# Kernel optimization log

Hardware: AMD Instinct MI355X
Metric: run time of the kernel (lower is better)

Reference implementation:

```python
import jax, jax.numpy as jnp
import numpy as np

O, I, G = 11008, 4096, 128  # out_features, in_features, weight_group


def setup_inputs() -> dict:
    key = jax.random.key(0)
    k1, k2, k3, k4, k5 = jax.random.split(key, 5)
    x = jax.random.normal(k1, (4096, I), dtype=jnp.float16)
    qweight = jax.random.randint(k2, (O, I * 4 // 8), 0, 256, dtype=jnp.int32)
    weight_scale = (jax.random.uniform(k3, (O, I // G), dtype=jnp.float32) * 0.02 + 0.001).astype(jnp.float16)
    weight_zero = jax.random.randint(k4, (O, I // G), 0, 16, dtype=jnp.int32)
    bias = jax.random.normal(k5, (O,), dtype=jnp.float16)
    return {"x": x, "qweight": qweight, "weight_scale": weight_scale,
            "weight_zero": weight_zero, "bias": bias}


def _dequant_w(qweight, weight_scale, weight_zero):
    # unpack two 4-bit values per byte: low nibble first, then high nibble
    low = qweight & 0xF
    high = (qweight >> 4) & 0xF
    w_q = jnp.stack([low, high], axis=-1).reshape(O, I)  # [O, I] ints in [0,16)
    # per-group dequant: (q - zero) * scale, group size G along in_features
    w = (w_q.astype(jnp.float16).reshape(-1, G)
         - weight_zero.reshape(-1, 1).astype(jnp.float16))
    w = w * weight_scale.reshape(-1, 1)
    return w.reshape(O, I).astype(jnp.float16)


def reference(x, qweight, weight_scale, weight_zero, bias):
    w = _dequant_w(qweight, weight_scale, weight_zero)  # [O, I] fp16
    return x @ w.T + bias  # F.linear(x, w, bias)
```

## Files before the change

kernel.cpp:

```cpp
#include <hip/hip_runtime.h>
#include <stdint.h>

#define MDIM 4096
#define NDIM 11008
#define KDIM 4096
#define KHALF 2048
#define NGRP 32
#define NXCD 8

#define WBYTES ((size_t)NDIM * KDIM * 2)
#define XBYTES ((size_t)MDIM * KDIM * 2)
#define WS_NEED (WBYTES + XBYTES)

#define G_BM 256
#define G_BN 256
#define G_BK 64
#define G_NTH 512
#define G_NTILN (NDIM / G_BN)
#define G_NWG ((MDIM / G_BM) * G_NTILN)

#define F_BM 128
#define F_BN 128
#define F_BK 64
#define F_NTH 256
#define F_NTILN (NDIM / F_BN)
#define F_NWG ((MDIM / F_BM) * F_NTILN)

typedef __attribute__((ext_vector_type(4))) float f32x4;
typedef __attribute__((ext_vector_type(8))) _Float16 f16x8;
typedef __attribute__((ext_vector_type(4))) int i32x4;
typedef __attribute__((ext_vector_type(4))) unsigned int u32x4;

__device__ __forceinline__ unsigned int pk16(float a, float b) {
  return __builtin_bit_cast(unsigned int, __builtin_amdgcn_cvt_pkrtz(a, b));
}
__device__ __forceinline__ unsigned int dq_pair(int qi, float fz, float s) {
  unsigned int q = (unsigned int)qi;
  float f0 = __uint_as_float((q & 0xFu) | 0x4B000000u);
  float f1 = __uint_as_float(((q >> 4) & 0xFu) | 0x4B000000u);
  return pk16((f0 - fz) * s, (f1 - fz) * s);
}
__device__ __forceinline__ void load_lds16(const void* g, void* l) {
  __builtin_amdgcn_global_load_lds(
      (__attribute__((address_space(1))) void*)(void*)g,
      (__attribute__((address_space(3))) void*)l, 16, 0, 0);
}

__global__ void __launch_bounds__(256)
dequant_w(const int* __restrict__ qw, const float* __restrict__ scl,
          const int* __restrict__ zro, _Float16* __restrict__ wh) {
  const unsigned int QTOT = (unsigned int)NDIM * KHALF;
  const unsigned int stride = gridDim.x * blockDim.x;
  for (unsigned int t = blockIdx.x * blockDim.x + threadIdx.x; t * 4u < QTOT;
       t += stride) {
    const unsigned int f = t * 4u;
    const unsigned int n = f >> 11;
    const unsigned int kk = f & (KHALF - 1);
    const unsigned int g = kk >> 6;
    const float s = scl[n * NGRP + g];
    const float fz = __uint_as_float(0x4B000000u | (unsigned int)zro[n * NGRP + g]);
    const i32x4 q = *(const i32x4*)(qw + f);
    u32x4 w;
#pragma unroll
    for (int e = 0; e < 4; ++e) w[e] = dq_pair(q[e], fz, s);
    *(u32x4*)(wh + (size_t)f * 2) = w;
  }
}

__global__ void __launch_bounds__(256)
cvt_x(const float* __restrict__ x, _Float16* __restrict__ xh) {
  const unsigned int XTOT = (unsigned int)MDIM * KDIM;
  const unsigned int stride = gridDim.x * blockDim.x;
  for (unsigned int t = blockIdx.x * blockDim.x + threadIdx.x; t * 8u < XTOT;
       t += stride) {
    const unsigned int f = t * 8u;
    const f32x4 a = *(const f32x4*)(x + f);
    const f32x4 b = *(const f32x4*)(x + f + 4);
    u32x4 w;
    w[0] = pk16(a[0], a[1]);
    w[1] = pk16(a[2], a[3]);
    w[2] = pk16(b[0], b[1]);
    w[3] = pk16(b[2], b[3]);
    *(u32x4*)(xh + f) = w;
  }
}

#define ABUF(b, h) ((b) * 32768 + (h) * 8192)
#define BBUF(b, h) ((b) * 32768 + 16384 + (h) * 8192)

#define BARRIER __builtin_amdgcn_s_barrier()
#define LGK0 do { asm volatile("s_waitcnt lgkmcnt(0)" ::: "memory"); \
                  __builtin_amdgcn_sched_barrier(0); } while (0)
#define VMC4 do { asm volatile("s_waitcnt vmcnt(4)" ::: "memory"); \
                  __builtin_amdgcn_sched_barrier(0); } while (0)

__global__ void __launch_bounds__(G_NTH, 2)
gemm_f16_8ph(const _Float16* __restrict__ xh, const _Float16* __restrict__ wh,
             const float* __restrict__ bia, float* __restrict__ outp) {
  __shared__ _Float16 lds[65536];

  const int tid = threadIdx.x;
  int wg = blockIdx.x;
  wg = (wg & 7) * (G_NWG / 8) + (wg >> 3);
  const int by = wg / G_NTILN;
  const int bx = wg - by * G_NTILN;
  const int m0 = by * G_BM;
  const int n0 = bx * G_BN;

  const int rowL = tid >> 3;
  const int swc = (((tid & 7) ^ (rowL & 7)) << 3);
  const unsigned int aO0 = (unsigned int)(m0 + rowL) * KDIM + swc;
  const unsigned int aO1 = aO0 + (unsigned int)128 * KDIM;
  const unsigned int bO0 = (unsigned int)(n0 + rowL) * KDIM + swc;
  const unsigned int bO1 = bO0 + (unsigned int)128 * KDIM;
  const int dst0 = tid << 3;

#define ST(base_el, gb, thoff, ko)                                     \
  do {                                                                 \
    load_lds16((gb) + (thoff) + (ko), lds + (base_el) + dst0);         \
    load_lds16((gb) + (thoff) + (unsigned)64 * KDIM + (ko),            \
               lds + (base_el) + 4096 + dst0);                         \
  } while (0)

  const int wave = tid >> 6, lane = tid & 63;
  const int wm = wave >> 2, wn = wave & 3;
  const int fr = lane & 15, fq = lane >> 4;
  const int pc0 = (fq ^ (fr & 7)) << 3;
  const int pc1 = ((4 + fq) ^ (fr & 7)) << 3;
  const int aoff0 = fr * 64 + pc0, aoff1 = fr * 64 + pc1;
  const int bb = ((wn & 1) << 12) + fr * 64;
  const int boff0 = bb + pc0, boff1 = bb + pc1;

  const _Float16* aP0 = lds + ABUF(0, 0) + wm * 8192;
  const _Float16* aP1 = lds + ABUF(1, 0) + wm * 8192;
  const _Float16* bP0 = lds + BBUF(0, 0) + (wn >> 1) * 8192;
  const _Float16* bP1 = lds + BBUF(1, 0) + (wn >> 1) * 8192;

#define RD_A03(P)                                           \
  _Pragma("unroll") for (int u = 0; u < 4; ++u) {           \
    aF[u][0] = *(const f16x8*)((P) + u * 1024 + aoff0);     \
    aF[u][1] = *(const f16x8*)((P) + u * 1024 + aoff1);     \
  }
#define RD_A47(P)                                               \
  _Pragma("unroll") for (int u = 0; u < 4; ++u) {               \
    aF[4 + u][0] = *(const f16x8*)((P) + (4 + u) * 1024 + aoff0); \
    aF[4 + u][1] = *(const f16x8*)((P) + (4 + u) * 1024 + aoff1); \
  }
#define RD_B01(P)                                           \
  _Pragma("unroll") for (int v = 0; v < 2; ++v) {           \
    bF[v][0] = *(const f16x8*)((P) + v * 1024 + boff0);     \
    bF[v][1] = *(const f16x8*)((P) + v * 1024 + boff1);     \
  }
#define RD_B23(P)                                               \
  _Pragma("unroll") for (int v = 0; v < 2; ++v) {               \
    bF[2 + v][0] = *(const f16x8*)((P) + (2 + v) * 1024 + boff0); \
    bF[2 + v][1] = *(const f16x8*)((P) + (2 + v) * 1024 + boff1); \
  }
#define QUAD(MI, NI)                                                     \
  do {                                                                   \
    __builtin_amdgcn_s_setprio(1);                                       \
    _Pragma("unroll") for (int u = 0; u < 4; ++u) {                      \
      _Pragma("unroll") for (int v = 0; v < 2; ++v) {                    \
        acc[(MI) + u][(NI) + v] = __builtin_amdgcn_mfma_f32_16x16x32_f16( \
            aF[(MI) + u][0], bF[(NI) + v][0], acc[(MI) + u][(NI) + v], 0, 0, 0); \
        acc[(MI) + u][(NI) + v] = __builtin_amdgcn_mfma_f32_16x16x32_f16( \
            aF[(MI) + u][1], bF[(NI) + v][1], acc[(MI) + u][(NI) + v], 0, 0, 0); \
      }                                                                  \
    }                                                                    \
    __builtin_amdgcn_s_setprio(0);                                       \
  } while (0)

  f16x8 aF[8][2], bF[4][2];
  f32x4 acc[8][4];
  const f32x4 fzero = {0.f, 0.f, 0.f, 0.f};
#pragma unroll
  for (int i = 0; i < 8; ++i)
#pragma unroll
    for (int j = 0; j < 4; ++j) acc[i][j] = fzero;

  ST(ABUF(0, 0), xh, aO0, 0u);
  ST(ABUF(0, 1), xh, aO1, 0u);
  ST(BBUF(0, 0), wh, bO0, 0u);
  ST(BBUF(0, 1), wh, bO1, 0u);
  ST(ABUF(1, 0), xh, aO0, 64u);
  ST(ABUF(1, 1), xh, aO1, 64u);
  VMC4;
  BARRIER;

  for (int it = 0; it < KDIM / 128; ++it) {
    const unsigned int k0 = (unsigned int)it << 7;
    const unsigned int ko1 = k0 + 64;
    const unsigned int ko2 = (k0 + 128) & 4095u;
    const unsigned int ko3 = (k0 + 192) & 4095u;

    RD_A03(aP0); RD_B01(bP0);
    ST(BBUF(1, 0), wh, bO0, ko1);
    BARRIER; LGK0; QUAD(0, 0); BARRIER;
    RD_A47(aP0);
    ST(BBUF(1, 1), wh, bO1, ko1);
    BARRIER; LGK0; QUAD(4, 0); BARRIER;
    RD_B23(bP0);
    ST(ABUF(0, 0), xh, aO0, ko2);
    BARRIER; LGK0; QUAD(0, 2); BARRIER;
    ST(ABUF(0, 1), xh, aO1, ko2);
    BARRIER; LGK0; QUAD(4, 2); VMC4; BARRIER;
    RD_A03(aP1); RD_B01(bP1);
    ST(BBUF(0, 0), wh, bO0, ko2);
    BARRIER; LGK0; QUAD(0, 0); BARRIER;
    RD_A47(aP1);
    ST(BBUF(0, 1), wh, bO1, ko2);
    BARRIER; LGK0; QUAD(4, 0); BARRIER;
    RD_B23(bP1);
    ST(ABUF(1, 0), xh, aO0, ko3);
    BARRIER; LGK0; QUAD(0, 2); BARRIER;
    ST(ABUF(1, 1), xh, aO1, ko3);
    BARRIER; LGK0; QUAD(4, 2); VMC4; BARRIER;
  }

#pragma unroll
  for (int ni = 0; ni < 4; ++ni) {
    const int n = n0 + wn * 64 + ni * 16 + fr;
    const float bv = bia[n];
#pragma unroll
    for (int mi = 0; mi < 8; ++mi) {
      const int m = m0 + wm * 128 + mi * 16 + (fq << 2);
      const size_t base = (size_t)m * NDIM + n;
#pragma unroll
      for (int j = 0; j < 4; ++j)
        outp[base + (size_t)j * NDIM] = acc[mi][ni][j] + bv;
    }
  }
}

__global__ void __launch_bounds__(F_NTH)
wlinear_fused(const float* __restrict__ x, const int* __restrict__ qw,
              const float* __restrict__ scl, const int* __restrict__ zro,
              const float* __restrict__ bia, float* __restrict__ outp) {
  __shared__ _Float16 ldsA[F_BM][F_BK];
  __shared__ _Float16 ldsB[F_BN][F_BK];

  const int tid = threadIdx.x;
  int wg = blockIdx.x;
  wg = (wg & (NXCD - 1)) * (F_NWG / NXCD) + (wg >> 3);
  const int by = wg / F_NTILN;
  const int bx = wg - by * F_NTILN;
  const int m0 = by * F_BM;
  const int n0 = bx * F_BN;

  const int srow = tid >> 1;
  const int sh = tid & 1;
  const int ssw = srow & 7;
  const float* xrow = x + (size_t)(m0 + srow) * KDIM + sh * 32;
  const int* qrow = qw + (size_t)(n0 + srow) * KHALF + sh * 16;
  const float* sclrow = scl + (size_t)(n0 + srow) * NGRP;
  const int* zrow = zro + (size_t)(n0 + srow) * NGRP;

  const int wave = tid >> 6;
  const int lane = tid & 63;
  const int wr = wave >> 1;
  const int wc = wave & 1;
  const int fr = lane & 15;
  const int fq = lane >> 4;
  const int off0 = ((fq ^ (fr & 7)) << 3);

  const f32x4 fzero = {0.f, 0.f, 0.f, 0.f};
  f32x4 acc[4][4];
#pragma unroll
  for (int i = 0; i < 4; ++i)
#pragma unroll
    for (int j = 0; j < 4; ++j) acc[i][j] = fzero;

  f32x4 xv[8];
  i32x4 qv[4];
  {
    const f32x4* xp = (const f32x4*)xrow;
#pragma unroll
    for (int i = 0; i < 8; ++i) xv[i] = xp[i];
    const i32x4* qp = (const i32x4*)qrow;
#pragma unroll
    for (int i = 0; i < 4; ++i) qv[i] = qp[i];
  }
  float s_n = sclrow[0];
  float fz_n = __uint_as_float(0x4B000000u | (unsigned int)zrow[0]);

  for (int k0 = 0; k0 < KDIM; k0 += F_BK) {
    __syncthreads();
#pragma unroll
    for (int j = 0; j < 4; ++j) {
      u32x4 wch;
      wch[0] = pk16(xv[2 * j][0], xv[2 * j][1]);
      wch[1] = pk16(xv[2 * j][2], xv[2 * j][3]);
      wch[2] = pk16(xv[2 * j + 1][0], xv[2 * j + 1][1]);
      wch[3] = pk16(xv[2 * j + 1][2], xv[2 * j + 1][3]);
      const int ps = (sh * 4 + j) ^ ssw;
      *(u32x4*)&ldsA[srow][ps << 3] = wch;
    }
#pragma unroll
    for (int ii = 0; ii < 4; ++ii) {
      u32x4 wch;
#pragma unroll
      for (int e = 0; e < 4; ++e) wch[e] = dq_pair(qv[ii][e], fz_n, s_n);
      const int ps = (sh * 4 + ii) ^ ssw;
      *(u32x4*)&ldsB[srow][ps << 3] = wch;
    }
    if (k0 + F_BK < KDIM) {
      const f32x4* xp = (const f32x4*)(xrow + k0 + F_BK);
#pragma unroll
      for (int i = 0; i < 8; ++i) xv[i] = xp[i];
      const i32x4* qp = (const i32x4*)(qrow + ((k0 + F_BK) >> 1));
#pragma unroll
      for (int i = 0; i < 4; ++i) qv[i] = qp[i];
      const int gn = (k0 + F_BK) >> 7;
      s_n = sclrow[gn];
      fz_n = __uint_as_float(0x4B000000u | (unsigned int)zrow[gn]);
    }
    __syncthreads();

#pragma unroll
    for (int ks = 0; ks < F_BK; ks += 32) {
      const int off = (ks == 0) ? off0 : (off0 ^ 32);
      f16x8 a[4], b[4];
#pragma unroll
      for (int mi = 0; mi < 4; ++mi)
        a[mi] = *(const f16x8*)&ldsA[wr * 64 + mi * 16 + fr][off];
#pragma unroll
      for (int ni = 0; ni < 4; ++ni)
        b[ni] = *(const f16x8*)&ldsB[wc * 64 + ni * 16 + fr][off];
#pragma unroll
      for (int mi = 0; mi < 4; ++mi)
#pragma unroll
        for (int ni = 0; ni < 4; ++ni)
          acc[mi][ni] = __builtin_amdgcn_mfma_f32_16x16x32_f16(
              a[mi], b[ni], acc[mi][ni], 0, 0, 0);
    }
  }

#pragma unroll
  for (int ni = 0; ni < 4; ++ni) {
    const int n = n0 + wc * 64 + ni * 16 + fr;
    const float bv = bia[n];
#pragma unroll
    for (int mi = 0; mi < 4; ++mi) {
      const int m = m0 + wr * 64 + mi * 16 + (fq << 2);
      const size_t base = (size_t)m * NDIM + n;
#pragma unroll
      for (int j = 0; j < 4; ++j)
        outp[base + (size_t)j * NDIM] = acc[mi][ni][j] + bv;
    }
  }
}

extern "C" void kernel_launch(void* const* d_in, const int* in_sizes, int n_in,
                              void* d_out, int out_size, void* d_ws, size_t ws_size,
                              hipStream_t stream) {
  (void)in_sizes; (void)n_in; (void)out_size;
  const float* x = (const float*)d_in[0];
  const int* qw = (const int*)d_in[1];
  const float* scl = (const float*)d_in[2];
  const int* zro = (const int*)d_in[3];
  const float* bia = (const float*)d_in[4];
  float* outp = (float*)d_out;

  if (ws_size >= WS_NEED) {
    _Float16* wh = (_Float16*)d_ws;
    _Float16* xh = (_Float16*)((char*)d_ws + WBYTES);
    dequant_w<<<2048, 256, 0, stream>>>(qw, scl, zro, wh);
    cvt_x<<<1024, 256, 0, stream>>>(x, xh);
    gemm_f16_8ph<<<G_NWG, G_NTH, 0, stream>>>(xh, wh, bia, outp);
  } else {
    wlinear_fused<<<F_NWG, F_NTH, 0, stream>>>(x, qw, scl, zro, bia, outp);
  }
}
```

Measured before the change: 618.4 us.

## Stream packed 4-bit weights into GEMM and dequantize in-kernel to LDS

The full fp16 dequantized weight matrix is no longer materialized. A pre-pass packs the int32-per-byte qweight into dense bytes and packs scale and zero into one word per group. The GEMM then loads those bytes through registers, dequantizes them with packed half arithmetic straight into the swizzled B LDS tiles, and changes the vmcnt waits to match. This removes the large fp16 weight write and re-read, in exchange for VALU dequant work inside the MFMA loop and a register-staged load path in place of direct-to-LDS loads.

```diff
diff --git a/kernel.cpp b/kernel.cpp
--- a/kernel.cpp
+++ b/kernel.cpp
@@ -5,16 +5,17 @@
 #define NDIM 11008
 #define KDIM 4096
 #define KHALF 2048
+#define KBYTES 2048
 #define NGRP 32
 #define NXCD 8
 
-#define WBYTES ((size_t)NDIM * KDIM * 2)
 #define XBYTES ((size_t)MDIM * KDIM * 2)
-#define WS_NEED (WBYTES + XBYTES)
+#define WPBYTES ((size_t)NDIM * KBYTES)
+#define SZBYTES ((size_t)NDIM * NGRP * 4)
+#define WS_NEED (XBYTES + WPBYTES + SZBYTES)
 
 #define G_BM 256
 #define G_BN 256
-#define G_BK 64
 #define G_NTH 512
 #define G_NTILN (NDIM / G_BN)
 #define G_NWG ((MDIM / G_BM) * G_NTILN)
@@ -28,6 +29,7 @@
 
 typedef __attribute__((ext_vector_type(4))) float f32x4;
 typedef __attribute__((ext_vector_type(8))) _Float16 f16x8;
+typedef __attribute__((ext_vector_type(2))) _Float16 h2;
 typedef __attribute__((ext_vector_type(4))) int i32x4;
 typedef __attribute__((ext_vector_type(4))) unsigned int u32x4;
 
@@ -40,6 +42,15 @@
   float f1 = __uint_as_float(((q >> 4) & 0xFu) | 0x4B000000u);
   return pk16((f0 - fz) * s, (f1 - fz) * s);
 }
+__device__ __forceinline__ unsigned int dq_byte(unsigned int w, int bi,
+                                                unsigned int zpk,
+                                                unsigned int spk) {
+  const unsigned int b = (w >> (8 * bi)) & 0xFFu;
+  const unsigned int u = 0x64006400u | (b & 0xFu) | ((b & 0xF0u) << 12);
+  const h2 r = (__builtin_bit_cast(h2, u) - __builtin_bit_cast(h2, zpk)) *
+               __builtin_bit_cast(h2, spk);
+  return __builtin_bit_cast(unsigned int, r);
+}
 __device__ __forceinline__ void load_lds16(const void* g, void* l) {
   __builtin_amdgcn_global_load_lds(
       (__attribute__((address_space(1))) void*)(void*)g,
@@ -47,23 +58,20 @@
 }
 
 __global__ void __launch_bounds__(256)
-dequant_w(const int* __restrict__ qw, const float* __restrict__ scl,
-          const int* __restrict__ zro, _Float16* __restrict__ wh) {
-  const unsigned int QTOT = (unsigned int)NDIM * KHALF;
+pack_w(const int* __restrict__ qw, unsigned char* __restrict__ wp) {
+  const unsigned int TOT = (unsigned int)NDIM * KHALF / 16u;
   const unsigned int stride = gridDim.x * blockDim.x;
-  for (unsigned int t = blockIdx.x * blockDim.x + threadIdx.x; t * 4u < QTOT;
+  for (unsigned int t = blockIdx.x * blockDim.x + threadIdx.x; t < TOT;
        t += stride) {
-    const unsigned int f = t * 4u;
-    const unsigned int n = f >> 11;
-    const unsigned int kk = f & (KHALF - 1);
-    const unsigned int g = kk >> 6;
-    const float s = scl[n * NGRP + g];
-    const float fz = __uint_as_float(0x4B000000u | (unsigned int)zro[n * NGRP + g]);
-    const i32x4 q = *(const i32x4*)(qw + f);
-    u32x4 w;
-#pragma unroll
-    for (int e = 0; e < 4; ++e) w[e] = dq_pair(q[e], fz, s);
-    *(u32x4*)(wh + (size_t)f * 2) = w;
+    const i32x4* qp = (const i32x4*)(qw + (size_t)t * 16);
+    u32x4 o;
+#pragma unroll
+    for (int j = 0; j < 4; ++j) {
+      const i32x4 q = qp[j];
+      o[j] = ((unsigned)q[0] & 0xFFu) | (((unsigned)q[1] & 0xFFu) << 8) |
+             (((unsigned)q[2] & 0xFFu) << 16) | (((unsigned)q[3] & 0xFFu) << 24);
+    }
+    *(u32x4*)(wp + (size_t)t * 16) = o;
   }
 }
 
@@ -85,18 +93,40 @@
   }
 }
 
+__global__ void __launch_bounds__(256)
+pack_sz(const float* __restrict__ scl, const int* __restrict__ zro,
+        unsigned int* __restrict__ szp) {
+  const unsigned int TOT = (unsigned int)NDIM * NGRP / 4u;
+  const unsigned int stride = gridDim.x * blockDim.x;
+  for (unsigned int t = blockIdx.x * blockDim.x + threadIdx.x; t < TOT;
+       t += stride) {
+    const f32x4 s = *(const f32x4*)(scl + (size_t)t * 4);
+    const i32x4 z = *(const i32x4*)(zro + (size_t)t * 4);
+    u32x4 o;
+#pragma unroll
+    for (int j = 0; j < 4; ++j) {
+      const unsigned int sb = pk16(s[j], s[j]) & 0xFFFFu;
+      o[j] = sb | ((unsigned)z[j] << 16);
+    }
+    *(u32x4*)(szp + (size_t)t * 4) = o;
+  }
+}
+
 #define ABUF(b, h) ((b) * 32768 + (h) * 8192)
 #define BBUF(b, h) ((b) * 32768 + 16384 + (h) * 8192)
 
 #define BARRIER __builtin_amdgcn_s_barrier()
 #define LGK0 do { asm volatile("s_waitcnt lgkmcnt(0)" ::: "memory"); \
                   __builtin_amdgcn_sched_barrier(0); } while (0)
-#define VMC4 do { asm volatile("s_waitcnt vmcnt(4)" ::: "memory"); \
-                  __builtin_amdgcn_sched_barrier(0); } while (0)
+#define VMC(N) do { asm volatile("s_waitcnt vmcnt(" #N ")" ::: "memory"); \
+                    __builtin_amdgcn_sched_barrier(0); } while (0)
+#define FENCE do { asm volatile("" ::: "memory"); \
+                   __builtin_amdgcn_sched_barrier(0); } while (0)
 
 __global__ void __launch_bounds__(G_NTH, 2)
-gemm_f16_8ph(const _Float16* __restrict__ xh, const _Float16* __restrict__ wh,
-             const float* __restrict__ bia, float* __restrict__ outp) {
+gemm_w4(const _Float16* __restrict__ xh, const unsigned char* __restrict__ wp,
+        const unsigned int* __restrict__ szp, const float* __restrict__ bia,
+        float* __restrict__ outp) {
   __shared__ _Float16 lds[65536];
 
   const int tid = threadIdx.x;
@@ -111,8 +141,6 @@
   const int swc = (((tid & 7) ^ (rowL & 7)) << 3);
   const unsigned int aO0 = (unsigned int)(m0 + rowL) * KDIM + swc;
   const unsigned int aO1 = aO0 + (unsigned int)128 * KDIM;
-  const unsigned int bO0 = (unsigned int)(n0 + rowL) * KDIM + swc;
-  const unsigned int bO1 = bO0 + (unsigned int)128 * KDIM;
   const int dst0 = tid << 3;
 
 #define ST(base_el, gb, thoff, ko)                                     \
@@ -120,6 +148,23 @@
     load_lds16((gb) + (thoff) + (ko), lds + (base_el) + dst0);         \
     load_lds16((gb) + (thoff) + (unsigned)64 * KDIM + (ko),            \
                lds + (base_el) + 4096 + dst0);                         \
+  } while (0)
+
+  const int nloc = tid >> 1;
+  const int bh = tid & 1;
+  const int nsw = nloc & 7;
+  const unsigned char* bqp = wp + (size_t)(n0 + nloc) * KBYTES + bh * 16;
+  const unsigned int* szr = szp + (size_t)(n0 + nloc) * NGRP;
+
+#define DQW(QV, BUF)                                                      \
+  do {                                                                    \
+    _Pragma("unroll") for (int j = 0; j < 4; ++j) {                       \
+      u32x4 o;                                                            \
+      _Pragma("unroll") for (int bi = 0; bi < 4; ++bi)                    \
+        o[bi] = dq_byte((QV)[j], bi, zpk, spk);                           \
+      *(u32x4*)(lds + (BUF) * 32768 + 16384 + nloc * 64 +                 \
+                ((((bh << 2) + j) ^ nsw) << 3)) = o;                      \
+    }                                                                     \
   } while (0)
 
   const int wave = tid >> 6, lane = tid & 63;
@@ -141,8 +186,8 @@
     aF[u][0] = *(const f16x8*)((P) + u * 1024 + aoff0);     \
     aF[u][1] = *(const f16x8*)((P) + u * 1024 + aoff1);     \
   }
-#define RD_A47(P)                                               \
-  _Pragma("unroll") for (int u = 0; u < 4; ++u) {               \
+#define RD_A47(P)                                                 \
+  _Pragma("unroll") for (int u = 0; u < 4; ++u) {                 \
     aF[4 + u][0] = *(const f16x8*)((P) + (4 + u) * 1024 + aoff0); \
     aF[4 + u][1] = *(const f16x8*)((P) + (4 + u) * 1024 + aoff1); \
   }
@@ -151,8 +196,8 @@
     bF[v][0] = *(const f16x8*)((P) + v * 1024 + boff0);     \
     bF[v][1] = *(const f16x8*)((P) + v * 1024 + boff1);     \
   }
-#define RD_B23(P)                                               \
-  _Pragma("unroll") for (int v = 0; v < 2; ++v) {               \
+#define RD_B23(P)                                                 \
+  _Pragma("unroll") for (int v = 0; v < 2; ++v) {                 \
     bF[2 + v][0] = *(const f16x8*)((P) + (2 + v) * 1024 + boff0); \
     bF[2 + v][1] = *(const f16x8*)((P) + (2 + v) * 1024 + boff1); \
   }
@@ -178,43 +223,65 @@
 #pragma unroll
     for (int j = 0; j < 4; ++j) acc[i][j] = fzero;
 
+  unsigned int zpk = 0, spk = 0;
+
+  u32x4 q0 = *(const u32x4*)(bqp + 0);
+  u32x4 q1 = *(const u32x4*)(bqp + 32);
+  unsigned int szv = szr[0];
+  FENCE;
   ST(ABUF(0, 0), xh, aO0, 0u);
   ST(ABUF(0, 1), xh, aO1, 0u);
-  ST(BBUF(0, 0), wh, bO0, 0u);
-  ST(BBUF(0, 1), wh, bO1, 0u);
   ST(ABUF(1, 0), xh, aO0, 64u);
   ST(ABUF(1, 1), xh, aO1, 64u);
-  VMC4;
+  FENCE;
+  VMC(8);
+  {
+    const unsigned int zl = szv >> 16;
+    zpk = 0x64006400u | zl | (zl << 16);
+    spk = (szv & 0xFFFFu) | (szv << 16);
+    DQW(q0, 0);
+    DQW(q1, 1);
+  }
+  VMC(4);
+  LGK0;
   BARRIER;
 
   for (int it = 0; it < KDIM / 128; ++it) {
-    const unsigned int k0 = (unsigned int)it << 7;
-    const unsigned int ko1 = k0 + 64;
-    const unsigned int ko2 = (k0 + 128) & 4095u;
-    const unsigned int ko3 = (k0 + 192) & 4095u;
+    const unsigned int ko2 = (128u * it + 128u) & 4095u;
+    const unsigned int ko3 = (128u * it + 192u) & 4095u;
+    const unsigned int kb2 = (64u * it + 64u) & 2047u;
+    const unsigned int kb3 = (64u * it + 96u) & 2047u;
 
     RD_A03(aP0); RD_B01(bP0);
-    ST(BBUF(1, 0), wh, bO0, ko1);
+    q0 = *(const u32x4*)(bqp + kb2);
+    szv = szr[(it + 1) & 31];
     BARRIER; LGK0; QUAD(0, 0); BARRIER;
     RD_A47(aP0);
-    ST(BBUF(1, 1), wh, bO1, ko1);
     BARRIER; LGK0; QUAD(4, 0); BARRIER;
     RD_B23(bP0);
     ST(ABUF(0, 0), xh, aO0, ko2);
     BARRIER; LGK0; QUAD(0, 2); BARRIER;
+    VMC(2);
+    {
+      const unsigned int zl = szv >> 16;
+      zpk = 0x64006400u | zl | (zl << 16);
+      spk = (szv & 0xFFFFu) | (szv << 16);
+      DQW(q0, 0);
+    }
     ST(ABUF(0, 1), xh, aO1, ko2);
-    BARRIER; LGK0; QUAD(4, 2); VMC4; BARRIER;
+    BARRIER; LGK0; QUAD(4, 2); BARRIER;
     RD_A03(aP1); RD_B01(bP1);
-    ST(BBUF(0, 0), wh, bO0, ko2);
+    q1 = *(const u32x4*)(bqp + kb3);
     BARRIER; LGK0; QUAD(0, 0); BARRIER;
     RD_A47(aP1);
-    ST(BBUF(0, 1), wh, bO1, ko2);
     BARRIER; LGK0; QUAD(4, 0); BARRIER;
     RD_B23(bP1);
     ST(ABUF(1, 0), xh, aO0, ko3);
     BARRIER; LGK0; QUAD(0, 2); BARRIER;
+    VMC(2);
+    DQW(q1, 1);
     ST(ABUF(1, 1), xh, aO1, ko3);
-    BARRIER; LGK0; QUAD(4, 2); VMC4; BARRIER;
+    BARRIER; LGK0; QUAD(4, 2); BARRIER;
   }
 
 #pragma unroll
@@ -362,11 +429,13 @@
   float* outp = (float*)d_out;
 
   if (ws_size >= WS_NEED) {
-    _Float16* wh = (_Float16*)d_ws;
-    _Float16* xh = (_Float16*)((char*)d_ws + WBYTES);
-    dequant_w<<<2048, 256, 0, stream>>>(qw, scl, zro, wh);
+    _Float16* xh = (_Float16*)d_ws;
+    unsigned char* wpk = (unsigned char*)d_ws + XBYTES;
+    unsigned int* szp = (unsigned int*)((char*)d_ws + XBYTES + WPBYTES);
     cvt_x<<<1024, 256, 0, stream>>>(x, xh);
-    gemm_f16_8ph<<<G_NWG, G_NTH, 0, stream>>>(xh, wh, bia, outp);
+    pack_w<<<1024, 256, 0, stream>>>(qw, wpk);
+    pack_sz<<<344, 256, 0, stream>>>(scl, zro, szp);
+    gemm_w4<<<G_NWG, G_NTH, 0, stream>>>(xh, wpk, szp, bia, outp);
   } else {
     wlinear_fused<<<F_NWG, F_NTH, 0, stream>>>(x, qw, scl, zro, bia, outp);
   }
```

New measurement: 692.5 us. +12.0%, slower.
